# Performance work log

Measured on AMD Instinct MI355X. Metric: run time of the kernel, lower is better.

## Reference

```python
import jax, jax.numpy as jnp
import numpy as np

H, D, C, K, N, B = 16, 64, 1024, 256, 4096, 2

def setup_inputs() -> dict:
    key = jax.random.key(0)
    ks = jax.random.split(key, 10)
    s = lambda k, shp, fan: jax.random.normal(k, shp, jnp.float32) * (1.0 / np.sqrt(fan))
    return {
        "x": jax.random.normal(ks[0], (B, N, C), jnp.float32),
        "Wq": s(ks[1], (H, D, C), C),   # per-head Linear(channels->dim), no bias
        "Wk": s(ks[2], (H, D, C), C),
        "Wv": s(ks[3], (H, D, C), C),
        "We": s(ks[4], (H, K, N), N),   # E: Linear(input_size->dim_k)
        "bE": jnp.zeros((H, K), jnp.float32),
        "Wf": s(ks[5], (H, K, N), N),   # F: Linear(input_size->dim_k)
        "bF": jnp.zeros((H, K), jnp.float32),
        "Wo": s(ks[6], (C, H * D), H * D),
        "bo": jnp.zeros((C,), jnp.float32),
    }

def reference(x, Wq, Wk, Wv, We, bE, Wf, bF, Wo, bo):
    b, n, c = x.shape
    h, d = Wq.shape[0], Wq.shape[1]
    # per-head Q/K/V projections, vectorized over heads: [b,h,n,d]
    Q = jnp.einsum('bnc,hdc->bhnd', x, Wq)
    Kt = jnp.einsum('bnc,hdc->bhdn', x, Wk)   # K already transposed(1,2)
    Vt = jnp.einsum('bnc,hdc->bhdn', x, Wv)   # V transposed(1,2)
    # Linformer E/F low-rank projections along sequence axis -> [b,h,d,k]
    Ke = jnp.einsum('bhdn,hkn->bhdk', Kt, We) + bE[None, :, None, :]
    Vf = jnp.einsum('bhdn,hkn->bhdk', Vt, Wf) + bF[None, :, None, :]
    # scaled scores + softmax over low-rank dim k
    scores = jnp.einsum('bhnd,bhdk->bhnk', Q, Kt if False else Ke) / jnp.sqrt(jnp.asarray(d, x.dtype))
    P = jax.nn.softmax(scores, axis=-1)
    # P @ V_f^T  -> [b,h,n,d]
    out = jnp.einsum('bhnk,bhkd->bhnd', P, jnp.swapaxes(Vf, -1, -2))
    # concat heads -> [b,n,h*d]
    out = jnp.transpose(out, (0, 2, 1, 3)).reshape(b, n, h * d)
    out = jax.nn.gelu(out, approximate=False)
    return out @ Wo.T + bo
```

## Files before the change

kernel.cpp:

```cpp
#include <hip/hip_runtime.h>

typedef unsigned short u16;
typedef float f32x4 __attribute__((ext_vector_type(4)));
typedef short s16x8 __attribute__((ext_vector_type(8)));
typedef unsigned short u16x4 __attribute__((ext_vector_type(4)));

__device__ __forceinline__ u16 f2bf(float f) {
  union { float f; unsigned u; } v; v.f = f;
  unsigned r = v.u + 0x7FFFu + ((v.u >> 16) & 1u);
  return (u16)(r >> 16);
}

__device__ __forceinline__ void gload_lds16(const void* g, void* l) {
  __builtin_amdgcn_global_load_lds(
      (const __attribute__((address_space(1))) void*)g,
      (__attribute__((address_space(3))) void*)l, 16, 0, 0);
}

__global__ __launch_bounds__(256) void cast_f32_bf16(
    const float* __restrict__ src, u16* __restrict__ dst, int n4) {
  int i = blockIdx.x * 256 + threadIdx.x;
  if (i >= n4) return;
  f32x4 v = ((const f32x4*)src)[i];
  u16x4 o = { f2bf(v[0]), f2bf(v[1]), f2bf(v[2]), f2bf(v[3]) };
  ((u16x4*)dst)[i] = o;
}

template <int FINAL>
__global__ __launch_bounds__(512) void gemm_pipe(
    const u16* __restrict__ A, const u16* __restrict__ B,
    void* __restrict__ Cout, const float* __restrict__ bias,
    int K, int lda, int ldb, int ldc) {
  __shared__ char smem[4 * 8192 + 4 * 16384];
  char* sA = smem;
  char* sB = smem + 32768;
  const int tid = threadIdx.x;
  const int wid = tid >> 6, lane = tid & 63;
  const int lo = lane & 15, hi = lane >> 4;
  const int wm = wid >> 2, wn = wid & 3;
  const long brow = (long)blockIdx.y * 128;
  const long bcol = (long)blockIdx.x * 256;
  const int T = K >> 5;

  f32x4 acc[4][4] = {};

  const char* Ab = (const char*)(A + (size_t)brow * lda);
  const char* Bb = (const char*)(B + (size_t)bcol * ldb);
  const size_t ldab = (size_t)lda * 2, ldbb = (size_t)ldb * 2;

  const int aoff = wid * 1024 + lane * 16;
  const int arow = aoff >> 6, acb = aoff & 63;
  const char* asrc = Ab + (size_t)arow * ldab + (acb ^ ((arow & 3) << 4));
  const int boff0 = (wid * 2) * 1024 + lane * 16;
  const int brw0 = boff0 >> 6, bcb0 = boff0 & 63;
  const char* bsrc0 = Bb + (size_t)brw0 * ldbb + (bcb0 ^ ((brw0 & 3) << 4));
  const int boff1 = (wid * 2 + 1) * 1024 + lane * 16;
  const int brw1 = boff1 >> 6, bcb1 = boff1 & 63;
  const char* bsrc1 = Bb + (size_t)brw1 * ldbb + (bcb1 ^ ((brw1 & 3) << 4));

  int ra[4], rb[4];
#pragma unroll
  for (int m = 0; m < 4; ++m)
    ra[m] = (wm * 64 + m * 16 + lo) * 64 + ((hi * 16) ^ ((lo & 3) << 4));
#pragma unroll
  for (int n = 0; n < 4; ++n)
    rb[n] = (wn * 64 + n * 16 + lo) * 64 + ((hi * 16) ^ ((lo & 3) << 4));

#define STAGE(t)                                                         \
  {                                                                      \
    int s_ = (t) & 3;                                                    \
    size_t kb_ = (size_t)(t) << 6;                                       \
    gload_lds16(asrc + kb_, sA + s_ * 8192 + wid * 1024);                \
    gload_lds16(bsrc0 + kb_, sB + s_ * 16384 + wid * 2048);              \
    gload_lds16(bsrc1 + kb_, sB + s_ * 16384 + wid * 2048 + 1024);       \
  }

  STAGE(0); STAGE(1); STAGE(2);
  asm volatile("s_waitcnt vmcnt(6)" ::: "memory");
  __builtin_amdgcn_s_barrier();
  __builtin_amdgcn_sched_barrier(0);

  for (int t = 0; t < T; ++t) {
    const char* bufA = sA + (t & 3) * 8192;
    const char* bufB = sB + (t & 3) * 16384;
    s16x8 af[4], bf[4];
#pragma unroll
    for (int m = 0; m < 4; ++m) af[m] = *(const s16x8*)(bufA + ra[m]);
#pragma unroll
    for (int n = 0; n < 4; ++n) bf[n] = *(const s16x8*)(bufB + rb[n]);
    if (t + 3 < T) STAGE(t + 3);
    __builtin_amdgcn_s_setprio(1);
#pragma unroll
    for (int m = 0; m < 4; ++m)
#pragma unroll
      for (int n = 0; n < 4; ++n)
        acc[m][n] = __builtin_amdgcn_mfma_f32_16x16x32_bf16(af[m], bf[n], acc[m][n], 0, 0, 0);
    __builtin_amdgcn_s_setprio(0);
    int rem = T - 2 - t;
    if (rem >= 2)      asm volatile("s_waitcnt vmcnt(6)" ::: "memory");
    else if (rem == 1) asm volatile("s_waitcnt vmcnt(3)" ::: "memory");
    else               asm volatile("s_waitcnt vmcnt(0)" ::: "memory");
    __builtin_amdgcn_s_barrier();
    __builtin_amdgcn_sched_barrier(0);
  }
#undef STAGE

#pragma unroll
  for (int m = 0; m < 4; ++m) {
#pragma unroll
    for (int n = 0; n < 4; ++n) {
#pragma unroll
      for (int r = 0; r < 4; ++r) {
        size_t row = brow + wm * 64 + m * 16 + hi * 4 + r;
        size_t col = bcol + wn * 64 + n * 16 + lo;
        float v = acc[m][n][r];
        if (FINAL) ((float*)Cout)[row * ldc + col] = v + bias[col];
        else       ((u16*)Cout)[row * ldc + col] = f2bf(v);
      }
    }
  }
}

__global__ __launch_bounds__(256) void kevf_kernel(
    const float* __restrict__ We, const float* __restrict__ Wf,
    const u16* __restrict__ QKV, float* __restrict__ part) {
  __shared__ u16 Wa[64 * 32];
  __shared__ u16 Vt[64 * 32];
  const int type = blockIdx.z >> 2, ns = blockIdx.z & 3;
  const int bh = blockIdx.y, b = bh >> 4, h = bh & 15;
  const int kk0 = blockIdx.x * 64;
  const float* W = (type ? Wf : We) + ((size_t)(h * 256 + kk0)) * 4096;
  const int col0 = (type ? 2048 : 1024) + h * 64;
  const int tid = threadIdx.x, wid = tid >> 6, lane = tid & 63;
  const int lo = lane & 15, hi = lane >> 4;

  f32x4 acc[4] = {};

  const int nbeg = ns << 10, nend = nbeg + 1024;
  for (int n0 = nbeg; n0 < nend; n0 += 32) {
    {
      int r = tid >> 2, c8 = (tid & 3) * 8;
      const f32x4* wp = (const f32x4*)(W + (size_t)r * 4096 + n0 + c8);
      f32x4 v0 = wp[0], v1 = wp[1];
      s16x8 wv;
      wv[0] = (short)f2bf(v0[0]); wv[1] = (short)f2bf(v0[1]);
      wv[2] = (short)f2bf(v0[2]); wv[3] = (short)f2bf(v0[3]);
      wv[4] = (short)f2bf(v1[0]); wv[5] = (short)f2bf(v1[1]);
      wv[6] = (short)f2bf(v1[2]); wv[7] = (short)f2bf(v1[3]);
      *(s16x8*)((char*)Wa + r * 64 + ((c8 * 2) ^ ((r & 3) << 4))) = wv;
    }
    {
      int n = tid >> 3, dd0 = (tid & 7) * 8;
      s16x8 v = *(const s16x8*)(QKV + (size_t)(b * 4096 + n0 + n) * 3072 + col0 + dd0);
#pragma unroll
      for (int q = 0; q < 8; ++q) {
        int dd = dd0 + q;
        Vt[dd * 32 + (n ^ (((dd >> 3) & 3) << 3))] = (u16)v[q];
      }
    }
    __syncthreads();
    int rr = wid * 16 + lo;
    s16x8 a = *(const s16x8*)((const char*)Wa + rr * 64 + ((hi * 16) ^ ((rr & 3) << 4)));
#pragma unroll
    for (int dt = 0; dt < 4; ++dt) {
      int dd = dt * 16 + lo;
      s16x8 bv = *(const s16x8*)&Vt[dd * 32 + ((hi * 8) ^ (((dd >> 3) & 3) << 3))];
      acc[dt] = __builtin_amdgcn_mfma_f32_16x16x32_bf16(a, bv, acc[dt], 0, 0, 0);
    }
    __syncthreads();
  }
  const size_t pbase = ((size_t)((type * 32 + bh) * 4 + blockIdx.x) * 4 + ns) * 4096;
#pragma unroll
  for (int dt = 0; dt < 4; ++dt)
#pragma unroll
    for (int r = 0; r < 4; ++r) {
      int kkl = wid * 16 + hi * 4 + r;
      int dd = dt * 16 + lo;
      part[pbase + kkl * 64 + dd] = acc[dt][r];
    }
}

__global__ __launch_bounds__(256) void kevf_reduce(
    const float* __restrict__ part, const float* __restrict__ bE,
    const float* __restrict__ bF, u16* __restrict__ KeT, u16* __restrict__ Vf) {
  const int tb = blockIdx.x;
  const int type = tb >> 7, bh = (tb >> 2) & 31, kc = tb & 3;
  const int t = threadIdx.x;
  const int kkl = t >> 2, dd0 = (t & 3) * 16;
  const float* p = part + (size_t)tb * 16384 + kkl * 64 + dd0;
  f32x4 s[4];
#pragma unroll
  for (int j = 0; j < 4; ++j) s[j] = ((const f32x4*)p)[j];
#pragma unroll
  for (int ns = 1; ns < 4; ++ns)
#pragma unroll
    for (int j = 0; j < 4; ++j) {
      f32x4 v = ((const f32x4*)(p + ns * 4096))[j];
      s[j][0] += v[0]; s[j][1] += v[1]; s[j][2] += v[2]; s[j][3] += v[3];
    }
  const int kk = kc * 64 + kkl;
  const float bias = (type ? bF : bE)[(bh & 15) * 256 + kk];
  if (type == 0) {
    u16* o = KeT + ((size_t)bh * 256 + kk) * 64 + dd0;
#pragma unroll
    for (int j = 0; j < 4; ++j) {
      u16x4 w = { f2bf(s[j][0] + bias), f2bf(s[j][1] + bias),
                  f2bf(s[j][2] + bias), f2bf(s[j][3] + bias) };
      *(u16x4*)(o + j * 4) = w;
    }
  } else {
#pragma unroll
    for (int j = 0; j < 4; ++j)
#pragma unroll
      for (int e = 0; e < 4; ++e) {
        int dd = dd0 + j * 4 + e;
        Vf[((size_t)bh * 64 + dd) * 256 + kk] = f2bf(s[j][e] + bias);
      }
  }
}

__global__ __launch_bounds__(256) void attn_fused(
    const u16* __restrict__ QKV, const u16* __restrict__ KeT,
    const u16* __restrict__ Vf, u16* __restrict__ attn) {
  __shared__ char smem[65536];
  char* sKe = smem;
  char* sVf = smem + 32768;
  const int tid = threadIdx.x, wid = tid >> 6, lane = tid & 63;
  const int lo = lane & 15, hi = lane >> 4;
  const int bh = blockIdx.y, b = bh >> 4, h = bh & 15;
  const int n0 = blockIdx.x * 64;

  const char* keg = (const char*)(KeT + (size_t)bh * 256 * 64);
  const char* vfg = (const char*)(Vf + (size_t)bh * 64 * 256);
#pragma unroll
  for (int i = 0; i < 8; ++i) {
    int ob = wid * 8192 + i * 1024;
    int o = ob + lane * 16;
    int kr = o >> 7, kc = o & 127;
    gload_lds16(keg + kr * 128 + (kc ^ ((kr & 7) << 4)), sKe + ob);
    int vr = o >> 9, vc = o & 511;
    gload_lds16(vfg + vr * 512 + (vc ^ ((vr & 7) << 4)), sVf + ob);
  }
  const u16* qp = QKV + (size_t)(b * 4096 + n0 + wid * 16 + lo) * 3072 + h * 64;
  s16x8 qf0 = *(const s16x8*)(qp + hi * 8);
  s16x8 qf1 = *(const s16x8*)(qp + 32 + hi * 8);
  __syncthreads();

  f32x4 sc[16];
#pragma unroll
  for (int nt = 0; nt < 16; ++nt) {
    int kk = nt * 16 + lo;
    int sw = (kk & 7) << 4;
    s16x8 b0 = *(const s16x8*)(sKe + kk * 128 + ((hi * 16) ^ sw));
    s16x8 b1 = *(const s16x8*)(sKe + kk * 128 + ((64 + hi * 16) ^ sw));
    f32x4 c = {0.f, 0.f, 0.f, 0.f};
    c = __builtin_amdgcn_mfma_f32_16x16x32_bf16(qf0, b0, c, 0, 0, 0);
    c = __builtin_amdgcn_mfma_f32_16x16x32_bf16(qf1, b1, c, 0, 0, 0);
    sc[nt] = c;
  }
  float mx[4], inv[4];
#pragma unroll
  for (int r = 0; r < 4; ++r) {
    float m = sc[0][r];
#pragma unroll
    for (int nt = 1; nt < 16; ++nt) m = fmaxf(m, sc[nt][r]);
    m = fmaxf(m, __shfl_xor(m, 1));
    m = fmaxf(m, __shfl_xor(m, 2));
    m = fmaxf(m, __shfl_xor(m, 4));
    m = fmaxf(m, __shfl_xor(m, 8));
    mx[r] = m;
  }
  const float SCL = 0.125f * 1.4426950408889634f;
  float sm[4] = {0.f, 0.f, 0.f, 0.f};
#pragma unroll
  for (int nt = 0; nt < 16; ++nt)
#pragma unroll
    for (int r = 0; r < 4; ++r) {
      float p = exp2f((sc[nt][r] - mx[r]) * SCL);
      sc[nt][r] = p;
      sm[r] += p;
    }
#pragma unroll
  for (int r = 0; r < 4; ++r) {
    float s = sm[r];
    s += __shfl_xor(s, 1);
    s += __shfl_xor(s, 2);
    s += __shfl_xor(s, 4);
    s += __shfl_xor(s, 8);
    inv[r] = 1.0f / s;
  }
  __syncthreads();
  char* pb = smem + wid * 8192;
#pragma unroll
  for (int nt = 0; nt < 16; ++nt)
#pragma unroll
    for (int r = 0; r < 4; ++r) {
      int row = hi * 4 + r;
      int kk = nt * 16 + lo;
      *(u16*)(pb + row * 512 + ((kk * 2) ^ ((row & 7) << 4))) = f2bf(sc[nt][r] * inv[r]);
    }
  __syncthreads();
  s16x8 pa[8];
#pragma unroll
  for (int ks = 0; ks < 8; ++ks)
    pa[ks] = *(const s16x8*)(pb + lo * 512 + ((ks * 64 + hi * 16) ^ ((lo & 7) << 4)));
#pragma unroll
  for (int dt = 0; dt < 4; ++dt) {
    int dd = dt * 16 + lo;
    int sw = (dd & 7) << 4;
    f32x4 o = {0.f, 0.f, 0.f, 0.f};
#pragma unroll
    for (int ks = 0; ks < 8; ++ks) {
      s16x8 vb = *(const s16x8*)(sVf + dd * 512 + ((ks * 64 + hi * 16) ^ sw));
      o = __builtin_amdgcn_mfma_f32_16x16x32_bf16(pa[ks], vb, o, 0, 0, 0);
    }
#pragma unroll
    for (int r = 0; r < 4; ++r) {
      int row = n0 + wid * 16 + hi * 4 + r;
      float x = o[r];
      float g = 0.5f * x * (1.0f + erff(x * 0.7071067811865476f));
      attn[(size_t)(b * 4096 + row) * 1024 + h * 64 + dd] = f2bf(g);
    }
  }
}

extern "C" void kernel_launch(void* const* d_in, const int* in_sizes, int n_in,
                              void* d_out, int out_size, void* d_ws, size_t ws_size,
                              hipStream_t stream) {
  const float* x  = (const float*)d_in[0];
  const float* Wq = (const float*)d_in[1];
  const float* Wk = (const float*)d_in[2];
  const float* Wv = (const float*)d_in[3];
  const float* We = (const float*)d_in[4];
  const float* bE = (const float*)d_in[5];
  const float* Wf = (const float*)d_in[6];
  const float* bF = (const float*)d_in[7];
  const float* Wo = (const float*)d_in[8];
  const float* bo = (const float*)d_in[9];
  float* out = (float*)d_out;

  char* ws = (char*)d_ws;
  u16* xb   = (u16*)(ws);
  u16* Wqkv = (u16*)(ws + 16777216);
  u16* Wob  = (u16*)(ws + 23068672);
  u16* QKV  = (u16*)(ws + 25165824);
  u16* KeT  = (u16*)(ws + 75497472);
  u16* Vf   = (u16*)(ws + 76546048);
  u16* attn = (u16*)(ws + 77594624);
  float* part = (float*)(ws);

  cast_f32_bf16<<<8192, 256, 0, stream>>>(x, xb, 2097152);
  cast_f32_bf16<<<1024, 256, 0, stream>>>(Wq, Wqkv, 262144);
  cast_f32_bf16<<<1024, 256, 0, stream>>>(Wk, Wqkv + 1048576, 262144);
  cast_f32_bf16<<<1024, 256, 0, stream>>>(Wv, Wqkv + 2097152, 262144);
  cast_f32_bf16<<<1024, 256, 0, stream>>>(Wo, Wob, 262144);

  gemm_pipe<0><<<dim3(12, 64), 512, 0, stream>>>(xb, Wqkv, QKV, nullptr,
                                                 1024, 1024, 1024, 3072);
  kevf_kernel<<<dim3(4, 32, 8), 256, 0, stream>>>(We, Wf, QKV, part);
  kevf_reduce<<<256, 256, 0, stream>>>(part, bE, bF, KeT, Vf);
  attn_fused<<<dim3(64, 32), 256, 0, stream>>>(QKV, KeT, Vf, attn);
  gemm_pipe<1><<<dim3(4, 64), 512, 0, stream>>>(attn, Wob, out, bo,
                                                1024, 1024, 1024, 1024);
}
```

Before: 220.9 us.

## Double-buffer kevf_kernel LDS and prefetch global loads two tiles ahead

Restructures the Linformer E/F projection kernel into a software pipeline. Global loads for the We/Wf rows and the V/K slice are issued into registers two tiles ahead, and LDS is double-buffered so one barrier per tile replaces two. Explicit vmcnt waits gate staging. The goal is to hide global load latency behind MFMA work, at the cost of more registers and LDS.

Measured after the change: 216.4 us. -2.0%, faster.

```diff
diff --git a/kernel.cpp b/kernel.cpp
--- a/kernel.cpp
+++ b/kernel.cpp
@@ -124,8 +124,8 @@
 __global__ __launch_bounds__(256) void kevf_kernel(
     const float* __restrict__ We, const float* __restrict__ Wf,
     const u16* __restrict__ QKV, float* __restrict__ part) {
-  __shared__ u16 Wa[64 * 32];
-  __shared__ u16 Vt[64 * 32];
+  __shared__ u16 Wa[2][64 * 32];
+  __shared__ u16 Vt[2][64 * 32];
   const int type = blockIdx.z >> 2, ns = blockIdx.z & 3;
   const int bh = blockIdx.y, b = bh >> 4, h = bh & 15;
   const int kk0 = blockIdx.x * 64;
@@ -133,50 +133,83 @@
   const int col0 = (type ? 2048 : 1024) + h * 64;
   const int tid = threadIdx.x, wid = tid >> 6, lane = tid & 63;
   const int lo = lane & 15, hi = lane >> 4;
+  const int nbeg = ns << 10;
+
+  const int r = tid >> 2, c8 = (tid & 3) * 8;
+  const int n = tid >> 3, dd0 = (tid & 7) * 8;
+  const float* Wrow = W + (size_t)r * 4096 + nbeg + c8;
+  const u16* Qrow = QKV + (size_t)(b * 4096 + nbeg + n) * 3072 + col0 + dd0;
+  const int wslot = r * 64 + ((c8 * 2) ^ ((r & 3) << 4));
+  const int rr = wid * 16 + lo;
+  const int raoff = rr * 64 + ((hi * 16) ^ ((rr & 3) << 4));
 
   f32x4 acc[4] = {};
-
-  const int nbeg = ns << 10, nend = nbeg + 1024;
-  for (int n0 = nbeg; n0 < nend; n0 += 32) {
-    {
-      int r = tid >> 2, c8 = (tid & 3) * 8;
-      const f32x4* wp = (const f32x4*)(W + (size_t)r * 4096 + n0 + c8);
-      f32x4 v0 = wp[0], v1 = wp[1];
-      s16x8 wv;
-      wv[0] = (short)f2bf(v0[0]); wv[1] = (short)f2bf(v0[1]);
-      wv[2] = (short)f2bf(v0[2]); wv[3] = (short)f2bf(v0[3]);
-      wv[4] = (short)f2bf(v1[0]); wv[5] = (short)f2bf(v1[1]);
-      wv[6] = (short)f2bf(v1[2]); wv[7] = (short)f2bf(v1[3]);
-      *(s16x8*)((char*)Wa + r * 64 + ((c8 * 2) ^ ((r & 3) << 4))) = wv;
-    }
-    {
-      int n = tid >> 3, dd0 = (tid & 7) * 8;
-      s16x8 v = *(const s16x8*)(QKV + (size_t)(b * 4096 + n0 + n) * 3072 + col0 + dd0);
-#pragma unroll
-      for (int q = 0; q < 8; ++q) {
-        int dd = dd0 + q;
-        Vt[dd * 32 + (n ^ (((dd >> 3) & 3) << 3))] = (u16)v[q];
-      }
-    }
+  f32x4 wA0, wA1, wB0, wB1;
+  s16x8 qA, qB;
+
+#define KISSUE(t, W0, W1, Q)                                        \
+  { const float* wp_ = Wrow + (size_t)(t) * 32;                     \
+    W0 = *(const f32x4*)wp_;                                        \
+    W1 = *(const f32x4*)(wp_ + 4);                                  \
+    Q = *(const s16x8*)(Qrow + (size_t)(t) * 32 * 3072); }
+
+#define KSTAGE(bf_, W0, W1, Q)                                      \
+  { s16x8 wv;                                                       \
+    wv[0] = (short)f2bf(W0[0]); wv[1] = (short)f2bf(W0[1]);         \
+    wv[2] = (short)f2bf(W0[2]); wv[3] = (short)f2bf(W0[3]);         \
+    wv[4] = (short)f2bf(W1[0]); wv[5] = (short)f2bf(W1[1]);         \
+    wv[6] = (short)f2bf(W1[2]); wv[7] = (short)f2bf(W1[3]);         \
+    *(s16x8*)((char*)Wa[bf_] + wslot) = wv;                         \
+    _Pragma("unroll")                                               \
+    for (int q = 0; q < 8; ++q) {                                   \
+      int dd = dd0 + q;                                             \
+      Vt[bf_][dd * 32 + (n ^ (((dd >> 3) & 3) << 3))] = (u16)Q[q];  \
+    } }
+
+#define KCOMPUTE(bf_)                                               \
+  { s16x8 a = *(const s16x8*)((const char*)Wa[bf_] + raoff);        \
+    _Pragma("unroll")                                               \
+    for (int dt = 0; dt < 4; ++dt) {                                \
+      int dd = dt * 16 + lo;                                        \
+      s16x8 bv = *(const s16x8*)&Vt[bf_][dd * 32 + ((hi * 8) ^ (((dd >> 3) & 3) << 3))]; \
+      acc[dt] = __builtin_amdgcn_mfma_f32_16x16x32_bf16(a, bv, acc[dt], 0, 0, 0); \
+    } }
+
+  KISSUE(0, wA0, wA1, qA);
+  KISSUE(1, wB0, wB1, qB);
+#pragma unroll 1
+  for (int tp = 0; tp < 15; ++tp) {
+    asm volatile("s_waitcnt vmcnt(3)" ::: "memory");
+    KSTAGE(0, wA0, wA1, qA);
     __syncthreads();
-    int rr = wid * 16 + lo;
-    s16x8 a = *(const s16x8*)((const char*)Wa + rr * 64 + ((hi * 16) ^ ((rr & 3) << 4)));
-#pragma unroll
-    for (int dt = 0; dt < 4; ++dt) {
+    KISSUE(2 * tp + 2, wA0, wA1, qA);
+    KCOMPUTE(0);
+    asm volatile("s_waitcnt vmcnt(3)" ::: "memory");
+    KSTAGE(1, wB0, wB1, qB);
+    __syncthreads();
+    KISSUE(2 * tp + 3, wB0, wB1, qB);
+    KCOMPUTE(1);
+  }
+  asm volatile("s_waitcnt vmcnt(3)" ::: "memory");
+  KSTAGE(0, wA0, wA1, qA);
+  __syncthreads();
+  KCOMPUTE(0);
+  asm volatile("s_waitcnt vmcnt(0)" ::: "memory");
+  KSTAGE(1, wB0, wB1, qB);
+  __syncthreads();
+  KCOMPUTE(1);
+#undef KISSUE
+#undef KSTAGE
+#undef KCOMPUTE
+
+  const size_t pbase = ((size_t)((type * 32 + bh) * 4 + blockIdx.x) * 4 + ns) * 4096;
+#pragma unroll
+  for (int dt = 0; dt < 4; ++dt)
+#pragma unroll
+    for (int rg = 0; rg < 4; ++rg) {
+      int kkl = wid * 16 + hi * 4 + rg;
       int dd = dt * 16 + lo;
-      s16x8 bv = *(const s16x8*)&Vt[dd * 32 + ((hi * 8) ^ (((dd >> 3) & 3) << 3))];
-      acc[dt] = __builtin_amdgcn_mfma_f32_16x16x32_bf16(a, bv, acc[dt], 0, 0, 0);
-    }
-    __syncthreads();
-  }
-  const size_t pbase = ((size_t)((type * 32 + bh) * 4 + blockIdx.x) * 4 + ns) * 4096;
-#pragma unroll
-  for (int dt = 0; dt < 4; ++dt)
-#pragma unroll
-    for (int r = 0; r < 4; ++r) {
-      int kkl = wid * 16 + hi * 4 + r;
-      int dd = dt * 16 + lo;
-      part[pbase + kkl * 64 + dd] = acc[dt][r];
+      part[pbase + kkl * 64 + dd] = acc[dt][rg];
     }
 }
 
```
